# Kernel tuning notes

Measured on AMD Instinct MI355X. Metric: run time of the kernel, lower is better.

The kernel has to match this reference:

```python
import jax, jax.numpy as jnp
import numpy as np

N_NODES = 10000
N_EDGES = 320000
D_FEAT = 128


def setup_inputs() -> dict:
    key = jax.random.key(0)
    k1, k2 = jax.random.split(key)
    feats = jax.random.normal(k1, (N_NODES, D_FEAT), dtype=jnp.float32)
    edge_index = jax.random.randint(k2, (2, N_EDGES), 0, N_NODES, dtype=jnp.int64)
    return {"feats": feats, "edge_index": edge_index}


def reference(feats, edge_index):
    # feats: [N, D]; edge_index: [2, E] with row 0 = src (u), row 1 = dst (v)
    src, dst = edge_index[0], edge_index[1]
    # u_sub_v gather-diff, abs-sum over feature dim, exp(-1/100 * .)
    diff_l1 = jnp.sum(jnp.abs(feats[src] - feats[dst]), axis=-1)  # [E]
    e = jnp.exp(-0.01 * diff_l1)[:, None]                          # [E, 1] (feats viewed [N,1,D])
    # edge_softmax: numerically-stable softmax over incoming edges of each dst node
    seg_max = jax.ops.segment_max(e, dst, num_segments=N_NODES)    # [N, 1]
    ex = jnp.exp(e - seg_max[dst])                                 # [E, 1]
    seg_sum = jax.ops.segment_sum(ex, dst, num_segments=N_NODES)   # [N, 1]
    return ex / seg_sum[dst]                                       # [E, 1]
```

## Files before the change

kernel.cpp:

```cpp
#include <hip/hip_runtime.h>
#include <hip/hip_fp16.h>

#define D_FEAT 128

__global__ void convert_kernel(const float* __restrict__ feats,
                               __half* __restrict__ feats16,
                               float* __restrict__ seg_sum,
                               int total8, int N) {
    int i = blockIdx.x * blockDim.x + threadIdx.x;
    if (i < N) seg_sum[i] = 0.0f;
    if (i >= total8) return;
    float4 v0 = ((const float4*)feats)[2 * i];
    float4 v1 = ((const float4*)feats)[2 * i + 1];
    __half2 h[4];
    h[0] = __floats2half2_rn(v0.x, v0.y);
    h[1] = __floats2half2_rn(v0.z, v0.w);
    h[2] = __floats2half2_rn(v1.x, v1.y);
    h[3] = __floats2half2_rn(v1.z, v1.w);
    ((uint4*)feats16)[i] = *reinterpret_cast<uint4*>(h);
}

__device__ inline float l1_u32(unsigned ua, unsigned ub) {
    __half2 ha = *reinterpret_cast<__half2*>(&ua);
    __half2 hb = *reinterpret_cast<__half2*>(&ub);
    float2 fa = __half22float2(ha);
    float2 fb = __half22float2(hb);
    return fabsf(fa.x - fb.x) + fabsf(fa.y - fb.y);
}
__device__ inline float l1_u4(uint4 a, uint4 b) {
    return l1_u32(a.x, b.x) + l1_u32(a.y, b.y)
         + l1_u32(a.z, b.z) + l1_u32(a.w, b.w);
}

__global__ void edge_eval_kernel(const __half* __restrict__ feats16,
                                 const int* __restrict__ src,
                                 const int* __restrict__ dst,
                                 float* __restrict__ seg_sum,
                                 float* __restrict__ out,
                                 int E) {
    int gtid = blockIdx.x * blockDim.x + threadIdx.x;
    int edge = gtid >> 3;
    int sl   = threadIdx.x & 7;
    if (edge >= E) return;

    int s = src[edge];
    int d = dst[edge];

    const uint4* fa = (const uint4*)(feats16 + (size_t)s * D_FEAT);
    const uint4* fb = (const uint4*)(feats16 + (size_t)d * D_FEAT);
    uint4 a0 = fa[sl];
    uint4 a1 = fa[sl + 8];
    uint4 b0 = fb[sl];
    uint4 b1 = fb[sl + 8];

    float sum = l1_u4(a0, b0) + l1_u4(a1, b1);

    #pragma unroll
    for (int off = 4; off >= 1; off >>= 1)
        sum += __shfl_xor(sum, off, 64);

    if (sl == 0) {
        float p = expf(expf(-0.01f * sum));
        out[edge] = p;
        atomicAdd(seg_sum + d, p);
    }
}

__global__ void edge_div_kernel(const int* __restrict__ dst,
                                const float* __restrict__ seg_sum,
                                float* __restrict__ out,
                                int E4) {
    int i = blockIdx.x * blockDim.x + threadIdx.x;
    if (i >= E4) return;
    float4 p = ((const float4*)out)[i];
    int4   d = ((const int4*)dst)[i];
    p.x /= seg_sum[d.x];
    p.y /= seg_sum[d.y];
    p.z /= seg_sum[d.z];
    p.w /= seg_sum[d.w];
    ((float4*)out)[i] = p;
}

__global__ void edge_div_tail_kernel(const int* __restrict__ dst,
                                     const float* __restrict__ seg_sum,
                                     float* __restrict__ out,
                                     int start, int E) {
    int e = start + blockIdx.x * blockDim.x + threadIdx.x;
    if (e >= E) return;
    out[e] = out[e] / seg_sum[dst[e]];
}

extern "C" void kernel_launch(void* const* d_in, const int* in_sizes, int n_in,
                              void* d_out, int out_size, void* d_ws, size_t ws_size,
                              hipStream_t stream) {
    const float* feats = (const float*)d_in[0];
    const int*   eidx  = (const int*)d_in[1];

    const int E = in_sizes[1] / 2;
    const int N = in_sizes[0] / D_FEAT;

    const int* src = eidx;
    const int* dst = eidx + E;

    float*  seg_sum = (float*)d_ws;
    __half* feats16 = (__half*)(seg_sum + ((N + 3) & ~3));
    float*  out     = (float*)d_out;

    {
        int total8 = N * D_FEAT / 8;
        dim3 blk(256);
        dim3 grd((total8 + 255) / 256);
        convert_kernel<<<grd, blk, 0, stream>>>(feats, feats16, seg_sum, total8, N);
    }
    {
        dim3 blk(256);
        dim3 grd((E + 31) / 32);
        edge_eval_kernel<<<grd, blk, 0, stream>>>(feats16, src, dst, seg_sum, out, E);
    }
    {
        int E4 = E >> 2;
        if (E4 > 0) {
            dim3 blk(256);
            dim3 grd((E4 + 255) / 256);
            edge_div_kernel<<<grd, blk, 0, stream>>>(dst, seg_sum, out, E4);
        }
        if (E & 3) {
            int start = E4 << 2;
            dim3 blk(64);
            dim3 grd(1);
            edge_div_tail_kernel<<<grd, blk, 0, stream>>>(dst, seg_sum, out, start, E);
        }
    }
}
```

Measured before the change: 41.37 us.

## Privatize segment sums into padded per-block-group copies to cut atomic contention

The per-destination atomicAdd accumulator is split into eight copies, each entry padded to 16 floats so entries land on separate cache lines, and blocks pick a copy by block index. A new reduce kernel folds the copies into a final total before the divide pass. The aim is to spread atomic traffic and avoid same-line contention, at the cost of an extra kernel launch, a much larger workspace (8*N*16 floats) and zeroing of every copy.

Result: faster. 37.74 us (-8.8%).

```diff
diff --git a/kernel.cpp b/kernel.cpp
--- a/kernel.cpp
+++ b/kernel.cpp
@@ -1,14 +1,19 @@
 #include <hip/hip_runtime.h>
 #include <hip/hip_fp16.h>
 
-#define D_FEAT 128
+#define D_FEAT  128
+#define PAD     16
+#define NCOPY   8
 
-__global__ void convert_kernel(const float* __restrict__ feats,
-                               __half* __restrict__ feats16,
-                               float* __restrict__ seg_sum,
-                               int total8, int N) {
+__global__ void convert_zero_kernel(const float* __restrict__ feats,
+                                    __half* __restrict__ feats16,
+                                    float* __restrict__ seg_copies,
+                                    int total8, int N) {
     int i = blockIdx.x * blockDim.x + threadIdx.x;
-    if (i < N) seg_sum[i] = 0.0f;
+    if (i < NCOPY * N) {
+        int c = i / N, n = i - c * N;
+        seg_copies[((size_t)c * N + n) * PAD] = 0.0f;
+    }
     if (i >= total8) return;
     float4 v0 = ((const float4*)feats)[2 * i];
     float4 v1 = ((const float4*)feats)[2 * i + 1];
@@ -35,9 +40,9 @@
 __global__ void edge_eval_kernel(const __half* __restrict__ feats16,
                                  const int* __restrict__ src,
                                  const int* __restrict__ dst,
-                                 float* __restrict__ seg_sum,
+                                 float* __restrict__ seg_copies,
                                  float* __restrict__ out,
-                                 int E) {
+                                 int E, int N) {
     int gtid = blockIdx.x * blockDim.x + threadIdx.x;
     int edge = gtid >> 3;
     int sl   = threadIdx.x & 7;
@@ -62,32 +67,44 @@
     if (sl == 0) {
         float p = expf(expf(-0.01f * sum));
         out[edge] = p;
-        atomicAdd(seg_sum + d, p);
+        float* copy = seg_copies + (size_t)(blockIdx.x & (NCOPY - 1)) * N * PAD;
+        atomicAdd(copy + (size_t)d * PAD, p);
     }
 }
 
+__global__ void reduce_kernel(const float* __restrict__ seg_copies,
+                              float* __restrict__ seg_tot, int N) {
+    int i = blockIdx.x * blockDim.x + threadIdx.x;
+    if (i >= N) return;
+    float s = 0.0f;
+    #pragma unroll
+    for (int c = 0; c < NCOPY; ++c)
+        s += seg_copies[((size_t)c * N + i) * PAD];
+    seg_tot[i] = s;
+}
+
 __global__ void edge_div_kernel(const int* __restrict__ dst,
-                                const float* __restrict__ seg_sum,
+                                const float* __restrict__ seg_tot,
                                 float* __restrict__ out,
                                 int E4) {
     int i = blockIdx.x * blockDim.x + threadIdx.x;
     if (i >= E4) return;
     float4 p = ((const float4*)out)[i];
     int4   d = ((const int4*)dst)[i];
-    p.x /= seg_sum[d.x];
-    p.y /= seg_sum[d.y];
-    p.z /= seg_sum[d.z];
-    p.w /= seg_sum[d.w];
+    p.x /= seg_tot[d.x];
+    p.y /= seg_tot[d.y];
+    p.z /= seg_tot[d.z];
+    p.w /= seg_tot[d.w];
     ((float4*)out)[i] = p;
 }
 
 __global__ void edge_div_tail_kernel(const int* __restrict__ dst,
-                                     const float* __restrict__ seg_sum,
+                                     const float* __restrict__ seg_tot,
                                      float* __restrict__ out,
                                      int start, int E) {
     int e = start + blockIdx.x * blockDim.x + threadIdx.x;
     if (e >= E) return;
-    out[e] = out[e] / seg_sum[dst[e]];
+    out[e] = out[e] / seg_tot[dst[e]];
 }
 
 extern "C" void kernel_launch(void* const* d_in, const int* in_sizes, int n_in,
@@ -102,33 +119,41 @@
     const int* src = eidx;
     const int* dst = eidx + E;
 
-    float*  seg_sum = (float*)d_ws;
-    __half* feats16 = (__half*)(seg_sum + ((N + 3) & ~3));
-    float*  out     = (float*)d_out;
+    float*  seg_copies = (float*)d_ws;
+    float*  seg_tot    = seg_copies + (size_t)NCOPY * N * PAD;
+    __half* feats16    = (__half*)(seg_tot + ((N + 3) & ~3));
+    float*  out        = (float*)d_out;
 
     {
         int total8 = N * D_FEAT / 8;
+        int work   = total8 > NCOPY * N ? total8 : NCOPY * N;
         dim3 blk(256);
-        dim3 grd((total8 + 255) / 256);
-        convert_kernel<<<grd, blk, 0, stream>>>(feats, feats16, seg_sum, total8, N);
+        dim3 grd((work + 255) / 256);
+        convert_zero_kernel<<<grd, blk, 0, stream>>>(feats, feats16,
+                                                     seg_copies, total8, N);
     }
     {
         dim3 blk(256);
         dim3 grd((E + 31) / 32);
-        edge_eval_kernel<<<grd, blk, 0, stream>>>(feats16, src, dst, seg_sum, out, E);
+        edge_eval_kernel<<<grd, blk, 0, stream>>>(feats16, src, dst,
+                                                  seg_copies, out, E, N);
+    }
+    {
+        dim3 blk(256);
+        dim3 grd((N + 255) / 256);
+        reduce_kernel<<<grd, blk, 0, stream>>>(seg_copies, seg_tot, N);
     }
     {
         int E4 = E >> 2;
         if (E4 > 0) {
             dim3 blk(256);
             dim3 grd((E4 + 255) / 256);
-            edge_div_kernel<<<grd, blk, 0, stream>>>(dst, seg_sum, out, E4);
+            edge_div_kernel<<<grd, blk, 0, stream>>>(dst, seg_tot, out, E4);
         }
         if (E & 3) {
             int start = E4 << 2;
-            dim3 blk(64);
-            dim3 grd(1);
-            edge_div_tail_kernel<<<grd, blk, 0, stream>>>(dst, seg_sum, out, start, E);
+            edge_div_tail_kernel<<<dim3(1), dim3(64), 0, stream>>>(
+                dst, seg_tot, out, start, E);
         }
     }
 }
```
